# Performance work log

Measured on AMD Instinct MI355X. Metric: run time of the kernel, lower is better.

## Reference

```python
import jax, jax.numpy as jnp
import numpy as np

DIM = 768
HEADS = 12
HEAD_DIM = DIM // HEADS
EPS_ATTN = 1e-6
LN_EPS = 1e-5


def _piece_weight():
    # BlockDistanceConv with num_patches_per_side=16, patch_group_size=16 -> 4x4 blocks
    bps = 4
    centers = np.array([[i + 0.5, j + 0.5] for i in range(bps) for j in range(bps)], dtype=np.float32)
    d = np.linalg.norm(centers[:, None, :] - centers[None, :, :], axis=-1)
    mat = np.cos(d / d.max() * np.pi / 4.0)  # 'cos' transform
    mat = mat / mat.sum(axis=0, keepdims=True)
    return jnp.asarray(mat, dtype=jnp.float32)  # [16, 16], out = W @ x over piece channels


def setup_inputs() -> dict:
    key = jax.random.key(0)
    ks = jax.random.split(key, 4)
    B, N, W, C = 128, 16, 16, DIM
    x = jax.random.normal(ks[0], (B, N, W, C), dtype=jnp.float32)
    ln_gamma = jnp.ones((C,), dtype=jnp.float32)
    ln_beta = jnp.zeros((C,), dtype=jnp.float32)
    w_qkv = jax.random.normal(ks[1], (C, 3 * C), dtype=jnp.float32) * (C ** -0.5)
    w_out = jax.random.normal(ks[2], (C, C), dtype=jnp.float32) * (C ** -0.5)
    b_out = jnp.zeros((C,), dtype=jnp.float32)
    w_piece = _piece_weight()
    return {"x": x, "ln_gamma": ln_gamma, "ln_beta": ln_beta, "w_qkv": w_qkv,
            "w_out": w_out, "b_out": b_out, "w_piece": w_piece}


def reference(x, ln_gamma, ln_beta, w_qkv, w_out, b_out, w_piece):
    B, N, W, C = x.shape
    H, D = HEADS, HEAD_DIM
    # LayerNorm over channel dim
    mu = jnp.mean(x, axis=-1, keepdims=True)
    var = jnp.mean((x - mu) ** 2, axis=-1, keepdims=True)
    xn = (x - mu) * jax.lax.rsqrt(var + LN_EPS) * ln_gamma + ln_beta
    # qkv projection (no bias)
    qkv = xn @ w_qkv  # [B,N,W,3C]
    q, k, v = jnp.split(qkv, 3, axis=-1)
    # relu kernel feature map
    q = jax.nn.relu(q) + EPS_ATTN
    k = jax.nn.relu(k) + EPS_ATTN
    # split heads: 'b n w (h d) -> b h n w d'
    def heads(t):
        return t.reshape(B, N, W, H, D).transpose(0, 3, 1, 2, 4)
    q, k, v = heads(q), heads(k), heads(v)
    # per-window kv = k^T v  (sum over window positions w)  -> [B,H,N,D,D]
    kv = jnp.einsum('bhnwd,bhnwe->bhnde', k, v)
    # BlockDistanceConv: 1x1 conv mixing over piece dim N with fixed weights
    kv = jnp.einsum('ij,bhjde->bhide', w_piece, kv)
    # out = q @ kv  -> [B,H,N,W,D]
    out = jnp.einsum('bhnwd,bhnde->bhnwe', q, kv)
    # merge heads: 'b h n w d -> b n w (h d)'
    out = out.transpose(0, 2, 3, 1, 4).reshape(B, N, W, H * D)
    # output projection (dropout is identity in eval)
    return out @ w_out + b_out
```

## Files before the change

kernel.cpp:

```cpp
#include <hip/hip_runtime.h>

#define DIM 768
#define HEADS 12
#define TOK 32768

typedef unsigned short ushort_t;
typedef __attribute__((ext_vector_type(8))) short short8v;
typedef __attribute__((ext_vector_type(4))) float f32x4;
typedef __attribute__((ext_vector_type(4))) unsigned short us4;

__device__ __forceinline__ ushort_t f2bf(float x) {
  union { float f; unsigned u; } c; c.f = x;
  unsigned r = (c.u + 0x7FFFu + ((c.u >> 16) & 1u)) >> 16;
  return (ushort_t)r;
}

__device__ __forceinline__ void gload_lds16(const void* g, void* l) {
  __builtin_amdgcn_global_load_lds((const __attribute__((address_space(1))) void*)g,
                                   (__attribute__((address_space(3))) void*)l, 16, 0, 0);
}

#define FENCE asm volatile("" ::: "memory")
#define SCHED0 __builtin_amdgcn_sched_barrier(0)
#define BARRIER do { FENCE; SCHED0; __builtin_amdgcn_s_barrier(); SCHED0; FENCE; } while (0)
#define LGK0 asm volatile("s_waitcnt lgkmcnt(0)" ::: "memory")

__global__ __launch_bounds__(256) void ln_kernel(const float* __restrict__ x,
                                                 const float* __restrict__ g,
                                                 const float* __restrict__ be,
                                                 ushort_t* __restrict__ xn) {
  int lane = threadIdx.x & 63;
  int row = blockIdx.x * 4 + (threadIdx.x >> 6);
  const float4* rx = (const float4*)(x + (size_t)row * DIM);
  float4 v[3];
  float s = 0.f, sq = 0.f;
  #pragma unroll
  for (int c = 0; c < 3; ++c) {
    v[c] = rx[lane + 64 * c];
    s  += v[c].x + v[c].y + v[c].z + v[c].w;
    sq += v[c].x * v[c].x + v[c].y * v[c].y + v[c].z * v[c].z + v[c].w * v[c].w;
  }
  #pragma unroll
  for (int off = 32; off; off >>= 1) {
    s  += __shfl_xor(s, off);
    sq += __shfl_xor(sq, off);
  }
  float mu  = s * (1.0f / DIM);
  float var = sq * (1.0f / DIM) - mu * mu;
  float rs  = rsqrtf(var + 1e-5f);
  us4* orow = (us4*)(xn + (size_t)row * DIM);
  const float4* gv = (const float4*)g;
  const float4* bv = (const float4*)be;
  #pragma unroll
  for (int c = 0; c < 3; ++c) {
    float4 gg = gv[lane + 64 * c];
    float4 bb = bv[lane + 64 * c];
    us4 pk;
    pk[0] = f2bf((v[c].x - mu) * rs * gg.x + bb.x);
    pk[1] = f2bf((v[c].y - mu) * rs * gg.y + bb.y);
    pk[2] = f2bf((v[c].z - mu) * rs * gg.z + bb.z);
    pk[3] = f2bf((v[c].w - mu) * rs * gg.w + bb.w);
    orow[lane + 64 * c] = pk;
  }
}

__global__ __launch_bounds__(256) void convT2(const float* __restrict__ s0,
                                              ushort_t* __restrict__ d0,
                                              const float* __restrict__ s1,
                                              ushort_t* __restrict__ d1) {
  int z = blockIdx.z;
  if (z && blockIdx.x >= DIM / 32) return;
  const float* src = z ? s1 : s0;
  ushort_t* dst = z ? d1 : d0;
  int Ccol = z ? DIM : 3 * DIM;
  const int R = DIM;
  __shared__ float tile[32][33];
  int c0 = blockIdx.x * 32, r0 = blockIdx.y * 32;
  int tx = threadIdx.x & 31, ty = threadIdx.x >> 5;
  #pragma unroll
  for (int i = 0; i < 32; i += 8)
    tile[ty + i][tx] = src[(size_t)(r0 + ty + i) * Ccol + c0 + tx];
  __syncthreads();
  #pragma unroll
  for (int i = 0; i < 32; i += 8)
    dst[(size_t)(c0 + ty + i) * R + r0 + tx] = f2bf(tile[tx][ty + i]);
}

__global__ __launch_bounds__(512, 2) void gemm_8ph(const ushort_t* __restrict__ A,
                                                   const ushort_t* __restrict__ Bt,
                                                   ushort_t* __restrict__ qbf,
                                                   ushort_t* __restrict__ kbf,
                                                   ushort_t* __restrict__ vTbf) {
  extern __shared__ __align__(16) char lds[];
  const int Kb = DIM * 2;
  const int N = 3 * DIM;
  const int nbn = N / 256;
  const size_t GHalf = (size_t)64 * Kb;

  int bid = blockIdx.x;
  int qd = gridDim.x >> 3;
  int wid = (bid & 7) * qd + (bid >> 3);
  int bm = wid / nbn, bn = wid % nbn;
  int row0 = bm * 256, col0 = bn * 256;
  int t = threadIdx.x;
  int lane = t & 63, wave = t >> 6;
  int wr = wave >> 2, wc = wave & 3;

  const char* Ag = (const char*)A + (size_t)row0 * Kb;
  const char* Bg = (const char*)Bt + (size_t)col0 * Kb;

  int o0 = t * 16;
  int sr = o0 >> 7;
  int skb = (o0 & 127) ^ ((sr & 7) << 4);
  size_t goff = (size_t)sr * Kb + skb;

  #define STG(Gbase, Lbase, kt)                                               \
    do {                                                                      \
      gload_lds16((Gbase) + goff + (size_t)(kt) * 128, lds + (Lbase) + o0);   \
      gload_lds16((Gbase) + goff + GHalf + (size_t)(kt) * 128,                \
                  lds + (Lbase) + o0 + 8192);                                 \
    } while (0)

  int fr = lane & 15, fkb = (lane >> 4) << 4;
  int swz = (fr & 7) << 4;
  int kb0 = fkb ^ swz;
  int kb1 = (64 + fkb) ^ swz;
  int laA = (wr * 128 + fr) * 128;
  int laB = 32768 + (wc * 64 + fr) * 128;

  #define LOAD_A(dst, dbase, mq)                                              \
    _Pragma("unroll") for (int mi = 0; mi < 4; ++mi) {                        \
      dst[mi][0] = *(const short8v*)(lds + (dbase) + laA + (mq)*8192 + mi*2048 + kb0); \
      dst[mi][1] = *(const short8v*)(lds + (dbase) + laA + (mq)*8192 + mi*2048 + kb1); \
    }
  #define LOAD_B(dst, dbase, nq)                                              \
    _Pragma("unroll") for (int ni = 0; ni < 2; ++ni) {                        \
      dst[ni][0] = *(const short8v*)(lds + (dbase) + laB + (nq)*4096 + ni*2048 + kb0); \
      dst[ni][1] = *(const short8v*)(lds + (dbase) + laB + (nq)*4096 + ni*2048 + kb1); \
    }
  #define MFMA16(av, bv, mq, nq)                                              \
    do {                                                                      \
      SCHED0;                                                                 \
      __builtin_amdgcn_s_setprio(1);                                          \
      _Pragma("unroll") for (int mi = 0; mi < 4; ++mi)                        \
        _Pragma("unroll") for (int ni = 0; ni < 2; ++ni) {                    \
          acc[(mq)*4+mi][(nq)*2+ni] = __builtin_amdgcn_mfma_f32_16x16x32_bf16(\
              av[mi][0], bv[ni][0], acc[(mq)*4+mi][(nq)*2+ni], 0, 0, 0);      \
          acc[(mq)*4+mi][(nq)*2+ni] = __builtin_amdgcn_mfma_f32_16x16x32_bf16(\
              av[mi][1], bv[ni][1], acc[(mq)*4+mi][(nq)*2+ni], 0, 0, 0);      \
        }                                                                     \
      __builtin_amdgcn_s_setprio(0);                                          \
    } while (0)

  STG(Ag, 0, 0);  STG(Ag + 128 * Kb, 16384, 0);
  STG(Bg, 32768, 0);  STG(Bg + 128 * Kb, 49152, 0);
  STG(Ag, 65536, 1);  STG(Ag + 128 * Kb, 65536 + 16384, 1);
  STG(Bg, 65536 + 32768, 1);
  asm volatile("s_waitcnt vmcnt(6)" ::: "memory");
  BARRIER;

  short8v aR0[4][2], aR1[4][2], bR0[2][2], bR1[2][2];
  LOAD_A(aR0, 0, 0); LOAD_B(bR0, 0, 0);

  f32x4 acc[8][4] = {};
  for (int it = 0; it < 6; ++it) {
    const int d0 = 0, d1 = 65536;
    int t1k = 2 * it + 1, t2k = 2 * it + 2, t3k = 2 * it + 3;
    bool st = (it < 5);
    LOAD_A(aR1, d0, 1);
    STG(Bg + 128 * Kb, d1 + 49152, t1k);
    MFMA16(aR0, bR0, 0, 0);
    BARRIER;
    LOAD_B(bR1, d0, 1);
    MFMA16(aR1, bR0, 1, 0);
    BARRIER;
    if (st) { STG(Ag, d0, t2k); STG(Ag + 128 * Kb, d0 + 16384, t2k); }
    MFMA16(aR0, bR1, 0, 1);
    if (st) asm volatile("s_waitcnt vmcnt(4)" ::: "memory");
    else    asm volatile("s_waitcnt vmcnt(0)" ::: "memory");
    BARRIER;
    LOAD_A(aR0, d1, 0); LOAD_B(bR0, d1, 0);
    if (st) STG(Bg, d0 + 32768, t2k);
    MFMA16(aR1, bR1, 1, 1);
    BARRIER;
    LOAD_A(aR1, d1, 1);
    if (st) STG(Bg + 128 * Kb, d0 + 49152, t2k);
    MFMA16(aR0, bR0, 0, 0);
    BARRIER;
    LOAD_B(bR1, d1, 1);
    MFMA16(aR1, bR0, 1, 0);
    BARRIER;
    if (st) { STG(Ag, d1, t3k); STG(Ag + 128 * Kb, d1 + 16384, t3k); }
    MFMA16(aR0, bR1, 0, 1);
    if (st) asm volatile("s_waitcnt vmcnt(4)" ::: "memory");
    BARRIER;
    if (st) {
      LOAD_A(aR0, d0, 0); LOAD_B(bR0, d0, 0);
      STG(Bg, d1 + 32768, t3k);
    }
    MFMA16(aR1, bR1, 1, 1);
    BARRIER;
  }
  #undef STG
  #undef LOAD_A
  #undef LOAD_B
  #undef MFMA16

  int rbase = row0 + wr * 128 + ((lane >> 4) << 2);
  int cbase = col0 + wc * 64 + fr;
  #pragma unroll
  for (int m = 0; m < 8; ++m) {
    int r0r = rbase + m * 16;
    #pragma unroll
    for (int n = 0; n < 4; ++n) {
      int c = cbase + n * 16;
      if (c < DIM) {
        #pragma unroll
        for (int j = 0; j < 4; ++j)
          qbf[(size_t)(r0r + j) * DIM + c] = f2bf(fmaxf(acc[m][n][j], 0.0f) + 1e-6f);
      } else if (c < 2 * DIM) {
        #pragma unroll
        for (int j = 0; j < 4; ++j)
          kbf[(size_t)(r0r + j) * DIM + (c - DIM)] = f2bf(fmaxf(acc[m][n][j], 0.0f) + 1e-6f);
      } else {
        int ch = c - 2 * DIM;
        int hh = ch >> 6, e = ch & 63;
        int bb = r0r >> 8, rr = r0r & 255;
        us4 pk;
        #pragma unroll
        for (int j = 0; j < 4; ++j) pk[j] = f2bf(acc[m][n][j]);
        *(us4*)&vTbf[((((size_t)bb * HEADS + hh) * 64 + e) << 8) + rr] = pk;
      }
    }
  }
}

__global__ __launch_bounds__(512, 2) void gemm_out8(const ushort_t* __restrict__ A,
                                                    const ushort_t* __restrict__ Bt,
                                                    const float* __restrict__ bias,
                                                    float* __restrict__ C) {
  extern __shared__ __align__(16) char lds[];
  const int Kb = DIM * 2;
  const int N = DIM;
  const int nbn = N / 128;
  const size_t GHalf = (size_t)64 * Kb;

  int bid = blockIdx.x;
  int qd = gridDim.x >> 3;
  int wid = (bid & 7) * qd + (bid >> 3);
  int bm = wid / nbn, bn = wid % nbn;
  int row0 = bm * 256, col0 = bn * 128;
  int t = threadIdx.x;
  int lane = t & 63, wave = t >> 6;
  int wr = wave >> 2, wc = wave & 3;

  const char* Ag = (const char*)A + (size_t)row0 * Kb;
  const char* Bg = (const char*)Bt + (size_t)col0 * Kb;

  int o0 = t * 16;
  int sr = o0 >> 7;
  int skb = (o0 & 127) ^ ((sr & 7) << 4);
  size_t goff = (size_t)sr * Kb + skb;

  #define STGA(Gbase, Lbase, kt)                                              \
    do {                                                                      \
      gload_lds16((Gbase) + goff + (size_t)(kt) * 128, lds + (Lbase) + o0);   \
      gload_lds16((Gbase) + goff + GHalf + (size_t)(kt) * 128,                \
                  lds + (Lbase) + o0 + 8192);                                 \
    } while (0)
  #define STGB(Gbase, Lbase, kt)                                              \
    gload_lds16((Gbase) + goff + (size_t)(kt) * 128, lds + (Lbase) + o0)

  int fr = lane & 15, fkb = (lane >> 4) << 4;
  int swz = (fr & 7) << 4;
  int kb0 = fkb ^ swz;
  int kb1 = (64 + fkb) ^ swz;
  int laA = (wr * 128 + fr) * 128;
  int laB = 32768 + (wc * 32 + fr) * 128;

  #define LOAD_A(dst, dbase, mq)                                              \
    _Pragma("unroll") for (int mi = 0; mi < 4; ++mi) {                        \
      dst[mi][0] = *(const short8v*)(lds + (dbase) + laA + (mq)*8192 + mi*2048 + kb0); \
      dst[mi][1] = *(const short8v*)(lds + (dbase) + laA + (mq)*8192 + mi*2048 + kb1); \
    }
  #define LOAD_B(dst, dbase, nq)                                              \
    do {                                                                      \
      dst[0] = *(const short8v*)(lds + (dbase) + laB + (nq)*2048 + kb0);      \
      dst[1] = *(const short8v*)(lds + (dbase) + laB + (nq)*2048 + kb1);      \
    } while (0)
  #define MFMA8(av, bv, mq, nq)                                               \
    do {                                                                      \
      SCHED0;                                                                 \
      __builtin_amdgcn_s_setprio(1);                                          \
      _Pragma("unroll") for (int mi = 0; mi < 4; ++mi) {                      \
        acc[(mq)*4+mi][nq] = __builtin_amdgcn_mfma_f32_16x16x32_bf16(         \
            av[mi][0], bv[0], acc[(mq)*4+mi][nq], 0, 0, 0);                   \
        acc[(mq)*4+mi][nq] = __builtin_amdgcn_mfma_f32_16x16x32_bf16(         \
            av[mi][1], bv[1], acc[(mq)*4+mi][nq], 0, 0, 0);                   \
      }                                                                       \
      __builtin_amdgcn_s_setprio(0);                                          \
    } while (0)

  STGA(Ag, 0, 0);  STGA(Ag + 128 * Kb, 16384, 0);
  STGB(Bg, 32768, 0);  STGB(Bg + GHalf, 32768 + 8192, 0);
  STGA(Ag, 49152, 1);  STGA(Ag + 128 * Kb, 49152 + 16384, 1);
  STGB(Bg, 49152 + 32768, 1);
  asm volatile("s_waitcnt vmcnt(5)" ::: "memory");
  BARRIER;

  short8v aR0[4][2], aR1[4][2], bR0[2], bR1[2];
  LOAD_A(aR0, 0, 0); LOAD_B(bR0, 0, 0);

  f32x4 acc[8][2] = {};
  for (int it = 0; it < 6; ++it) {
    const int d0 = 0, d1 = 49152;
    int t1k = 2 * it + 1, t2k = 2 * it + 2, t3k = 2 * it + 3;
    bool st = (it < 5);
    LOAD_A(aR1, d0, 1);
    STGB(Bg + GHalf, d1 + 32768 + 8192, t1k);
    MFMA8(aR0, bR0, 0, 0);
    BARRIER;
    LOAD_B(bR1, d0, 1);
    MFMA8(aR1, bR0, 1, 0);
    BARRIER;
    if (st) { STGA(Ag, d0, t2k); STGA(Ag + 128 * Kb, d0 + 16384, t2k); }
    MFMA8(aR0, bR1, 0, 1);
    if (st) asm volatile("s_waitcnt vmcnt(4)" ::: "memory");
    else    asm volatile("s_waitcnt vmcnt(0)" ::: "memory");
    BARRIER;
    LOAD_A(aR0, d1, 0); LOAD_B(bR0, d1, 0);
    if (st) STGB(Bg, d0 + 32768, t2k);
    MFMA8(aR1, bR1, 1, 1);
    BARRIER;
    LOAD_A(aR1, d1, 1);
    if (st) STGB(Bg + GHalf, d0 + 32768 + 8192, t2k);
    MFMA8(aR0, bR0, 0, 0);
    BARRIER;
    LOAD_B(bR1, d1, 1);
    MFMA8(aR1, bR0, 1, 0);
    BARRIER;
    if (st) { STGA(Ag, d1, t3k); STGA(Ag + 128 * Kb, d1 + 16384, t3k); }
    MFMA8(aR0, bR1, 0, 1);
    if (st) asm volatile("s_waitcnt vmcnt(4)" ::: "memory");
    BARRIER;
    if (st) {
      LOAD_A(aR0, d0, 0); LOAD_B(bR0, d0, 0);
      STGB(Bg, d1 + 32768, t3k);
    }
    MFMA8(aR1, bR1, 1, 1);
    BARRIER;
  }
  #undef STGA
  #undef STGB
  #undef LOAD_A
  #undef LOAD_B
  #undef MFMA8

  int rbase = row0 + wr * 128 + ((lane >> 4) << 2);
  int cbase = col0 + wc * 32 + fr;
  #pragma unroll
  for (int m = 0; m < 8; ++m) {
    #pragma unroll
    for (int n = 0; n < 2; ++n) {
      int c = cbase + n * 16;
      float bz = bias[c];
      #pragma unroll
      for (int j = 0; j < 4; ++j)
        C[(size_t)(rbase + m * 16 + j) * N + c] = acc[m][n][j] + bz;
    }
  }
}

__global__ __launch_bounds__(512) void attn_fused(const ushort_t* __restrict__ qbf,
                                                  const ushort_t* __restrict__ kbf,
                                                  const ushort_t* __restrict__ vTbf,
                                                  const float* __restrict__ wp,
                                                  ushort_t* __restrict__ attnO) {
  extern __shared__ __align__(16) char lds[];
  const int QOFF = 65536, SOFF = 73728;
  int bh = blockIdx.x;
  int b = bh / HEADS, h = bh % HEADS;
  int t = threadIdx.x;
  int lane = t & 63, wave = t >> 6;
  int fr = lane & 15, fkb = (lane >> 4) << 4;
  int lg4 = (lane >> 4) << 2;

  const char* qg = (const char*)(qbf + ((size_t)b * 256) * DIM + h * 64);
  const char* kg = (const char*)(kbf + ((size_t)b * 256) * DIM + h * 64);
  const char* vg = (const char*)(vTbf + ((size_t)bh << 14));

  #pragma unroll
  for (int is = 0; is < 4; ++is) {
    int o = is * 8192 + t * 16;
    int r = o >> 7;
    int byt = (o & 127) ^ ((r & 7) << 4);
    gload_lds16(kg + (size_t)r * (DIM * 2) + byt, lds + o);
  }
  {
    int o = t * 16;
    int r = o >> 7;
    int byt = (o & 127) ^ ((r & 7) << 4);
    gload_lds16(qg + (size_t)r * (DIM * 2) + byt, lds + QOFF + o);
  }
  #pragma unroll
  for (int is = 0; is < 4; ++is) {
    int o = is * 8192 + t * 16;
    int e = o >> 9;
    int byt = (o & 511) ^ ((e & 7) << 4);
    gload_lds16(vg + e * 512 + byt, lds + 32768 + o);
  }
  asm volatile("s_waitcnt vmcnt(4)" ::: "memory");
  __builtin_amdgcn_s_barrier();

  int wrs = wave & 3, wcs = wave >> 2;
  int wrp = wave >> 2, wcp = wave & 3;

  for (int q4 = 0; q4 < 4; ++q4) {
    f32x4 accA[4][2] = {};
    {
      short8v kf[4][2], qf[2][2];
      #pragma unroll
      for (int mi = 0; mi < 4; ++mi)
        #pragma unroll
        for (int ks = 0; ks < 2; ++ks) {
          int r = wrs * 64 + mi * 16 + fr;
          kf[mi][ks] = *(const short8v*)(lds + r * 128 + ((ks * 64 + fkb) ^ ((r & 7) << 4)));
        }
      #pragma unroll
      for (int ni = 0; ni < 2; ++ni)
        #pragma unroll
        for (int ks = 0; ks < 2; ++ks) {
          int r = wcs * 32 + ni * 16 + fr;
          qf[ni][ks] = *(const short8v*)(lds + QOFF + r * 128 + ((ks * 64 + fkb) ^ ((r & 7) << 4)));
        }
      #pragma unroll
      for (int mi = 0; mi < 4; ++mi)
        #pragma unroll
        for (int ni = 0; ni < 2; ++ni)
          #pragma unroll
          for (int ks = 0; ks < 2; ++ks)
            accA[mi][ni] = __builtin_amdgcn_mfma_f32_16x16x32_bf16(kf[mi][ks], qf[ni][ks],
                                                                   accA[mi][ni], 0, 0, 0);
    }
    BARRIER;
    #pragma unroll
    for (int mi = 0; mi < 4; ++mi)
      #pragma unroll
      for (int ni = 0; ni < 2; ++ni) {
        float wpf = wp[(q4 * 4 + wcs * 2 + ni) * 16 + wrs * 4 + mi];
        us4 pk;
        #pragma unroll
        for (int j = 0; j < 4; ++j) pk[j] = f2bf(accA[mi][ni][j] * wpf);
        int qrow = wcs * 32 + ni * 16 + fr;
        int sbyte = (wrs * 64 + mi * 16 + lg4) * 2;
        *(us4*)(lds + SOFF + qrow * 512 + (sbyte ^ ((qrow & 7) << 4))) = pk;
      }
    if (q4 < 3) {
      int o = t * 16;
      int r = o >> 7;
      int byt = (o & 127) ^ ((r & 7) << 4);
      gload_lds16(qg + (size_t)((q4 + 1) * 64 + r) * (DIM * 2) + byt, lds + QOFF + o);
    }
    LGK0;
    BARRIER;
    if (q4 == 0) asm volatile("s_waitcnt vmcnt(1)" ::: "memory");
    f32x4 accB[2] = {{0.f,0.f,0.f,0.f},{0.f,0.f,0.f,0.f}};
    #pragma unroll
    for (int ks = 0; ks < 8; ++ks) {
      int kb = ks * 64 + fkb;
      int e = wcp * 16 + fr;
      short8v bv = *(const short8v*)(lds + 32768 + e * 512 + (kb ^ ((e & 7) << 4)));
      #pragma unroll
      for (int mt = 0; mt < 2; ++mt) {
        int r = wrp * 32 + mt * 16 + fr;
        short8v av = *(const short8v*)(lds + SOFF + r * 512 + (kb ^ ((r & 7) << 4)));
        accB[mt] = __builtin_amdgcn_mfma_f32_16x16x32_bf16(av, bv, accB[mt], 0, 0, 0);
      }
    }
    #pragma unroll
    for (int mt = 0; mt < 2; ++mt) {
      int row = b * 256 + q4 * 64 + wrp * 32 + mt * 16 + lg4;
      int col = h * 64 + wcp * 16 + fr;
      #pragma unroll
      for (int j = 0; j < 4; ++j)
        attnO[(size_t)(row + j) * DIM + col] = f2bf(accB[mt][j]);
    }
    if (q4 < 3) asm volatile("s_waitcnt vmcnt(8)" ::: "memory");
    BARRIER;
  }
}

extern "C" void kernel_launch(void* const* d_in, const int* in_sizes, int n_in,
                              void* d_out, int out_size, void* d_ws, size_t ws_size,
                              hipStream_t stream) {
  const float* x    = (const float*)d_in[0];
  const float* g    = (const float*)d_in[1];
  const float* be   = (const float*)d_in[2];
  const float* wqkv = (const float*)d_in[3];
  const float* wout = (const float*)d_in[4];
  const float* bout = (const float*)d_in[5];
  const float* wp   = (const float*)d_in[6];
  float* out = (float*)d_out;

  char* w = (char*)d_ws;
  const size_t SZ = (size_t)TOK * DIM * 2;
  ushort_t* qbf   = (ushort_t*)(w);
  ushort_t* kbf   = (ushort_t*)(w + SZ);
  ushort_t* vTbf  = (ushort_t*)(w + 2 * SZ);
  ushort_t* xn    = (ushort_t*)(w + 3 * SZ);
  ushort_t* wqkvT = (ushort_t*)(w + 4 * SZ);
  ushort_t* woutT = (ushort_t*)(w + 4 * SZ + 3538944);
  ushort_t* attnO = xn;

  (void)hipFuncSetAttribute(reinterpret_cast<const void*>(&gemm_8ph),
                            hipFuncAttributeMaxDynamicSharedMemorySize, 131072);
  (void)hipFuncSetAttribute(reinterpret_cast<const void*>(&gemm_out8),
                            hipFuncAttributeMaxDynamicSharedMemorySize, 98304);
  (void)hipFuncSetAttribute(reinterpret_cast<const void*>(&attn_fused),
                            hipFuncAttributeMaxDynamicSharedMemorySize, 106496);

  dim3 gct(3 * DIM / 32, DIM / 32, 2);
  convT2<<<gct, 256, 0, stream>>>(wqkv, wqkvT, wout, woutT);

  ln_kernel<<<TOK / 4, 256, 0, stream>>>(x, g, be, xn);

  gemm_8ph<<<(TOK / 256) * (3 * DIM / 256), 512, 131072, stream>>>(
      xn, wqkvT, qbf, kbf, vTbf);

  attn_fused<<<128 * HEADS, 512, 106496, stream>>>(qbf, kbf, vTbf, wp, attnO);

  gemm_out8<<<(TOK / 256) * (DIM / 128), 512, 98304, stream>>>(
      attnO, woutT, bout, out);
}
```

Baseline: 288.1 us.

## Reschedule GEMM main loops with finer-grained staging and explicit waitcnt barriers

Restructures the software pipeline in both GEMM kernels (QKV and output projection). Each global-to-LDS stage is now split into one load per sub-step, and every LDS fragment load is followed by a barrier and an lgkmcnt wait before the MFMA block. The prologue preloads less data, and the barrier macro no longer carries scheduling barriers, so the compiler has more freedom to reorder. The aim is to spread memory traffic evenly across MFMA phases and shorten stalls, at the cost of more barriers per iteration.

```diff
diff --git a/kernel.cpp b/kernel.cpp
--- a/kernel.cpp
+++ b/kernel.cpp
@@ -22,8 +22,11 @@
 
 #define FENCE asm volatile("" ::: "memory")
 #define SCHED0 __builtin_amdgcn_sched_barrier(0)
-#define BARRIER do { FENCE; SCHED0; __builtin_amdgcn_s_barrier(); SCHED0; FENCE; } while (0)
+#define BAR do { FENCE; __builtin_amdgcn_s_barrier(); FENCE; } while (0)
 #define LGK0 asm volatile("s_waitcnt lgkmcnt(0)" ::: "memory")
+#define LGK8 asm volatile("s_waitcnt lgkmcnt(8)" ::: "memory")
+#define VM2  asm volatile("s_waitcnt vmcnt(2)" ::: "memory")
+#define VM0  asm volatile("s_waitcnt vmcnt(0)" ::: "memory")
 
 __global__ __launch_bounds__(256) void ln_kernel(const float* __restrict__ x,
                                                  const float* __restrict__ g,
@@ -140,7 +143,6 @@
     }
   #define MFMA16(av, bv, mq, nq)                                              \
     do {                                                                      \
-      SCHED0;                                                                 \
       __builtin_amdgcn_s_setprio(1);                                          \
       _Pragma("unroll") for (int mi = 0; mi < 4; ++mi)                        \
         _Pragma("unroll") for (int ni = 0; ni < 2; ++ni) {                    \
@@ -150,56 +152,63 @@
               av[mi][1], bv[ni][1], acc[(mq)*4+mi][(nq)*2+ni], 0, 0, 0);      \
         }                                                                     \
       __builtin_amdgcn_s_setprio(0);                                          \
+      SCHED0;                                                                 \
     } while (0)
 
   STG(Ag, 0, 0);  STG(Ag + 128 * Kb, 16384, 0);
   STG(Bg, 32768, 0);  STG(Bg + 128 * Kb, 49152, 0);
-  STG(Ag, 65536, 1);  STG(Ag + 128 * Kb, 65536 + 16384, 1);
-  STG(Bg, 65536 + 32768, 1);
-  asm volatile("s_waitcnt vmcnt(6)" ::: "memory");
-  BARRIER;
-
-  short8v aR0[4][2], aR1[4][2], bR0[2][2], bR1[2][2];
-  LOAD_A(aR0, 0, 0); LOAD_B(bR0, 0, 0);
+  STG(Ag, 65536, 1);
+  VM2;
+  BAR;
 
   f32x4 acc[8][4] = {};
+  short8v A0[4][2], A1[4][2], B0[2][2], B1[2][2];
   for (int it = 0; it < 6; ++it) {
     const int d0 = 0, d1 = 65536;
-    int t1k = 2 * it + 1, t2k = 2 * it + 2, t3k = 2 * it + 3;
+    int todd = 2 * it + 1, tev = 2 * it + 2, todd3 = 2 * it + 3;
     bool st = (it < 5);
-    LOAD_A(aR1, d0, 1);
-    STG(Bg + 128 * Kb, d1 + 49152, t1k);
-    MFMA16(aR0, bR0, 0, 0);
-    BARRIER;
-    LOAD_B(bR1, d0, 1);
-    MFMA16(aR1, bR0, 1, 0);
-    BARRIER;
-    if (st) { STG(Ag, d0, t2k); STG(Ag + 128 * Kb, d0 + 16384, t2k); }
-    MFMA16(aR0, bR1, 0, 1);
-    if (st) asm volatile("s_waitcnt vmcnt(4)" ::: "memory");
-    else    asm volatile("s_waitcnt vmcnt(0)" ::: "memory");
-    BARRIER;
-    LOAD_A(aR0, d1, 0); LOAD_B(bR0, d1, 0);
-    if (st) STG(Bg, d0 + 32768, t2k);
-    MFMA16(aR1, bR1, 1, 1);
-    BARRIER;
-    LOAD_A(aR1, d1, 1);
-    if (st) STG(Bg + 128 * Kb, d0 + 49152, t2k);
-    MFMA16(aR0, bR0, 0, 0);
-    BARRIER;
-    LOAD_B(bR1, d1, 1);
-    MFMA16(aR1, bR0, 1, 0);
-    BARRIER;
-    if (st) { STG(Ag, d1, t3k); STG(Ag + 128 * Kb, d1 + 16384, t3k); }
-    MFMA16(aR0, bR1, 0, 1);
-    if (st) asm volatile("s_waitcnt vmcnt(4)" ::: "memory");
-    BARRIER;
-    if (st) {
-      LOAD_A(aR0, d0, 0); LOAD_B(bR0, d0, 0);
-      STG(Bg, d1 + 32768, t3k);
-    }
-    MFMA16(aR1, bR1, 1, 1);
-    BARRIER;
+    LOAD_A(A0, d0, 0); LOAD_B(B0, d0, 0);
+    STG(Ag + 128 * Kb, d1 + 16384, todd);
+    LGK8;
+    BAR; LGK0; SCHED0;
+    MFMA16(A0, B0, 0, 0);
+    BAR;
+    LOAD_A(A1, d0, 1);
+    STG(Bg, d1 + 32768, todd);
+    BAR; LGK0; SCHED0;
+    MFMA16(A1, B0, 1, 0);
+    BAR;
+    LOAD_B(B1, d0, 1);
+    STG(Bg + 128 * Kb, d1 + 49152, todd);
+    BAR; LGK0; SCHED0;
+    MFMA16(A0, B1, 0, 1);
+    BAR;
+    if (st) STG(Ag, d0, tev);
+    BAR; SCHED0;
+    MFMA16(A1, B1, 1, 1);
+    if (st) VM2; else VM0;
+    BAR;
+    LOAD_A(A0, d1, 0); LOAD_B(B0, d1, 0);
+    if (st) STG(Ag + 128 * Kb, d0 + 16384, tev);
+    LGK8;
+    BAR; LGK0; SCHED0;
+    MFMA16(A0, B0, 0, 0);
+    BAR;
+    LOAD_A(A1, d1, 1);
+    if (st) STG(Bg, d0 + 32768, tev);
+    BAR; LGK0; SCHED0;
+    MFMA16(A1, B0, 1, 0);
+    BAR;
+    LOAD_B(B1, d1, 1);
+    if (st) STG(Bg + 128 * Kb, d0 + 49152, tev);
+    BAR; LGK0; SCHED0;
+    MFMA16(A0, B1, 0, 1);
+    BAR;
+    if (st) STG(Ag, d1, todd3);
+    BAR; SCHED0;
+    MFMA16(A1, B1, 1, 1);
+    if (st) VM2;
+    BAR;
   }
   #undef STG
   #undef LOAD_A
@@ -290,7 +299,6 @@
     } while (0)
   #define MFMA8(av, bv, mq, nq)                                               \
     do {                                                                      \
-      SCHED0;                                                                 \
       __builtin_amdgcn_s_setprio(1);                                          \
       _Pragma("unroll") for (int mi = 0; mi < 4; ++mi) {                      \
         acc[(mq)*4+mi][nq] = __builtin_amdgcn_mfma_f32_16x16x32_bf16(         \
@@ -299,56 +307,61 @@
             av[mi][1], bv[1], acc[(mq)*4+mi][nq], 0, 0, 0);                   \
       }                                                                       \
       __builtin_amdgcn_s_setprio(0);                                          \
+      SCHED0;                                                                 \
     } while (0)
 
   STGA(Ag, 0, 0);  STGA(Ag + 128 * Kb, 16384, 0);
-  STGB(Bg, 32768, 0);  STGB(Bg + GHalf, 32768 + 8192, 0);
-  STGA(Ag, 49152, 1);  STGA(Ag + 128 * Kb, 49152 + 16384, 1);
-  STGB(Bg, 49152 + 32768, 1);
-  asm volatile("s_waitcnt vmcnt(5)" ::: "memory");
-  BARRIER;
-
-  short8v aR0[4][2], aR1[4][2], bR0[2], bR1[2];
-  LOAD_A(aR0, 0, 0); LOAD_B(bR0, 0, 0);
+  STGB(Bg, 32768, 0);  STGB(Bg + GHalf, 40960, 0);
+  STGA(Ag, 49152, 1);
+  VM2;
+  BAR;
 
   f32x4 acc[8][2] = {};
+  short8v A0[4][2], A1[4][2], B0[2], B1[2];
   for (int it = 0; it < 6; ++it) {
     const int d0 = 0, d1 = 49152;
-    int t1k = 2 * it + 1, t2k = 2 * it + 2, t3k = 2 * it + 3;
+    int todd = 2 * it + 1, tev = 2 * it + 2, todd3 = 2 * it + 3;
     bool st = (it < 5);
-    LOAD_A(aR1, d0, 1);
-    STGB(Bg + GHalf, d1 + 32768 + 8192, t1k);
-    MFMA8(aR0, bR0, 0, 0);
-    BARRIER;
-    LOAD_B(bR1, d0, 1);
-    MFMA8(aR1, bR0, 1, 0);
-    BARRIER;
-    if (st) { STGA(Ag, d0, t2k); STGA(Ag + 128 * Kb, d0 + 16384, t2k); }
-    MFMA8(aR0, bR1, 0, 1);
-    if (st) asm volatile("s_waitcnt vmcnt(4)" ::: "memory");
-    else    asm volatile("s_waitcnt vmcnt(0)" ::: "memory");
-    BARRIER;
-    LOAD_A(aR0, d1, 0); LOAD_B(bR0, d1, 0);
-    if (st) STGB(Bg, d0 + 32768, t2k);
-    MFMA8(aR1, bR1, 1, 1);
-    BARRIER;
-    LOAD_A(aR1, d1, 1);
-    if (st) STGB(Bg + GHalf, d0 + 32768 + 8192, t2k);
-    MFMA8(aR0, bR0, 0, 0);
-    BARRIER;
-    LOAD_B(bR1, d1, 1);
-    MFMA8(aR1, bR0, 1, 0);
-    BARRIER;
-    if (st) { STGA(Ag, d1, t3k); STGA(Ag + 128 * Kb, d1 + 16384, t3k); }
-    MFMA8(aR0, bR1, 0, 1);
-    if (st) asm volatile("s_waitcnt vmcnt(4)" ::: "memory");
-    BARRIER;
-    if (st) {
-      LOAD_A(aR0, d0, 0); LOAD_B(bR0, d0, 0);
-      STGB(Bg, d1 + 32768, t3k);
-    }
-    MFMA8(aR1, bR1, 1, 1);
-    BARRIER;
+    LOAD_A(A0, d0, 0); LOAD_B(B0, d0, 0);
+    STGA(Ag + 128 * Kb, d1 + 16384, todd);
+    BAR; LGK0; SCHED0;
+    MFMA8(A0, B0, 0, 0);
+    BAR;
+    LOAD_A(A1, d0, 1);
+    STGB(Bg, d1 + 32768, todd);
+    BAR; LGK0; SCHED0;
+    MFMA8(A1, B0, 1, 0);
+    BAR;
+    LOAD_B(B1, d0, 1);
+    STGB(Bg + GHalf, d1 + 40960, todd);
+    BAR; LGK0; SCHED0;
+    MFMA8(A0, B1, 0, 1);
+    BAR;
+    if (st) STGA(Ag, d0, tev);
+    BAR; SCHED0;
+    MFMA8(A1, B1, 1, 1);
+    if (st) VM2; else VM0;
+    BAR;
+    LOAD_A(A0, d1, 0); LOAD_B(B0, d1, 0);
+    if (st) STGA(Ag + 128 * Kb, d0 + 16384, tev);
+    BAR; LGK0; SCHED0;
+    MFMA8(A0, B0, 0, 0);
+    BAR;
+    LOAD_A(A1, d1, 1);
+    if (st) STGB(Bg, d0 + 32768, tev);
+    BAR; LGK0; SCHED0;
+    MFMA8(A1, B0, 1, 0);
+    BAR;
+    LOAD_B(B1, d1, 1);
+    if (st) STGB(Bg + GHalf, d0 + 40960, tev);
+    BAR; LGK0; SCHED0;
+    MFMA8(A0, B1, 0, 1);
+    BAR;
+    if (st) STGA(Ag, d1, todd3);
+    BAR; SCHED0;
+    MFMA8(A1, B1, 1, 1);
+    if (st) VM2;
+    BAR;
   }
   #undef STGA
   #undef STGB
@@ -442,7 +455,7 @@
             accA[mi][ni] = __builtin_amdgcn_mfma_f32_16x16x32_bf16(kf[mi][ks], qf[ni][ks],
                                                                    accA[mi][ni], 0, 0, 0);
     }
-    BARRIER;
+    BAR;
     #pragma unroll
     for (int mi = 0; mi < 4; ++mi)
       #pragma unroll
@@ -462,7 +475,7 @@
       gload_lds16(qg + (size_t)((q4 + 1) * 64 + r) * (DIM * 2) + byt, lds + QOFF + o);
     }
     LGK0;
-    BARRIER;
+    BAR;
     if (q4 == 0) asm volatile("s_waitcnt vmcnt(1)" ::: "memory");
     f32x4 accB[2] = {{0.f,0.f,0.f,0.f},{0.f,0.f,0.f,0.f}};
     #pragma unroll
@@ -486,7 +499,7 @@
         attnO[(size_t)(row + j) * DIM + col] = f2bf(accB[mt][j]);
     }
     if (q4 < 3) asm volatile("s_waitcnt vmcnt(8)" ::: "memory");
-    BARRIER;
+    BAR;
   }
 }
 
```

After: 290.6 us. Within noise of the previous version (+0.9%).

## Shrink LDS footprint of output GEMM and attention kernels to raise occupancy

Applied to the files above, without the earlier changes.

The output GEMM drops its hand-tuned 8-phase, 128-byte-K pipeline for a simple double-buffered loop over 32-wide K tiles using 48KB of LDS, with a 4x2 wave grid holding 4x4 accumulators each and launch bounds asking for 4 blocks per CU. The attention kernel keeps V^T in registers, reusing the V LDS region as score scratch so its LDS shrinks to 72KB, and also asks for 4 blocks per CU. The goal is more resident blocks to hide latency, at the cost of losing the finer software pipelining, adding more barriers per K step and increasing register pressure.

```diff
diff --git a/kernel.cpp b/kernel.cpp
--- a/kernel.cpp
+++ b/kernel.cpp
@@ -24,6 +24,8 @@
 #define SCHED0 __builtin_amdgcn_sched_barrier(0)
 #define BARRIER do { FENCE; SCHED0; __builtin_amdgcn_s_barrier(); SCHED0; FENCE; } while (0)
 #define LGK0 asm volatile("s_waitcnt lgkmcnt(0)" ::: "memory")
+#define VM0  asm volatile("s_waitcnt vmcnt(0)" ::: "memory")
+#define VM3  asm volatile("s_waitcnt vmcnt(3)" ::: "memory")
 
 __global__ __launch_bounds__(256) void ln_kernel(const float* __restrict__ x,
                                                  const float* __restrict__ g,
@@ -235,7 +237,7 @@
   }
 }
 
-__global__ __launch_bounds__(512, 2) void gemm_out8(const ushort_t* __restrict__ A,
+__global__ __launch_bounds__(512, 4) void gemm_out8(const ushort_t* __restrict__ A,
                                                     const ushort_t* __restrict__ Bt,
                                                     const float* __restrict__ bias,
                                                     float* __restrict__ C) {
@@ -243,7 +245,7 @@
   const int Kb = DIM * 2;
   const int N = DIM;
   const int nbn = N / 128;
-  const size_t GHalf = (size_t)64 * Kb;
+  const int NT = DIM / 32;
 
   int bid = blockIdx.x;
   int qd = gridDim.x >> 3;
@@ -252,116 +254,65 @@
   int row0 = bm * 256, col0 = bn * 128;
   int t = threadIdx.x;
   int lane = t & 63, wave = t >> 6;
-  int wr = wave >> 2, wc = wave & 3;
+  int wr = wave >> 1, wc = wave & 1;
 
   const char* Ag = (const char*)A + (size_t)row0 * Kb;
   const char* Bg = (const char*)Bt + (size_t)col0 * Kb;
 
-  int o0 = t * 16;
-  int sr = o0 >> 7;
-  int skb = (o0 & 127) ^ ((sr & 7) << 4);
-  size_t goff = (size_t)sr * Kb + skb;
-
-  #define STGA(Gbase, Lbase, kt)                                              \
+  int oA0 = t * 16, oA1 = 8192 + t * 16;
+  int rA0 = oA0 >> 6, rA1 = oA1 >> 6;
+  size_t gA0 = (size_t)rA0 * Kb + ((oA0 & 63) ^ ((rA0 & 3) << 4));
+  size_t gA1 = (size_t)rA1 * Kb + ((oA1 & 63) ^ ((rA1 & 3) << 4));
+  int oB = t * 16;
+  int rB = oB >> 6;
+  size_t gB = (size_t)rB * Kb + ((oB & 63) ^ ((rB & 3) << 4));
+
+  #define STG2(tile, slot)                                                    \
     do {                                                                      \
-      gload_lds16((Gbase) + goff + (size_t)(kt) * 128, lds + (Lbase) + o0);   \
-      gload_lds16((Gbase) + goff + GHalf + (size_t)(kt) * 128,                \
-                  lds + (Lbase) + o0 + 8192);                                 \
+      char* sb = lds + (slot) * 24576;                                        \
+      size_t kk = (size_t)(tile) * 64;                                        \
+      gload_lds16(Ag + gA0 + kk, sb + oA0);                                   \
+      gload_lds16(Ag + gA1 + kk, sb + oA1);                                   \
+      gload_lds16(Bg + gB + kk, sb + 16384 + oB);                             \
     } while (0)
-  #define STGB(Gbase, Lbase, kt)                                              \
-    gload_lds16((Gbase) + goff + (size_t)(kt) * 128, lds + (Lbase) + o0)
 
   int fr = lane & 15, fkb = (lane >> 4) << 4;
-  int swz = (fr & 7) << 4;
-  int kb0 = fkb ^ swz;
-  int kb1 = (64 + fkb) ^ swz;
-  int laA = (wr * 128 + fr) * 128;
-  int laB = 32768 + (wc * 32 + fr) * 128;
-
-  #define LOAD_A(dst, dbase, mq)                                              \
-    _Pragma("unroll") for (int mi = 0; mi < 4; ++mi) {                        \
-      dst[mi][0] = *(const short8v*)(lds + (dbase) + laA + (mq)*8192 + mi*2048 + kb0); \
-      dst[mi][1] = *(const short8v*)(lds + (dbase) + laA + (mq)*8192 + mi*2048 + kb1); \
-    }
-  #define LOAD_B(dst, dbase, nq)                                              \
-    do {                                                                      \
-      dst[0] = *(const short8v*)(lds + (dbase) + laB + (nq)*2048 + kb0);      \
-      dst[1] = *(const short8v*)(lds + (dbase) + laB + (nq)*2048 + kb1);      \
-    } while (0)
-  #define MFMA8(av, bv, mq, nq)                                               \
-    do {                                                                      \
-      SCHED0;                                                                 \
-      __builtin_amdgcn_s_setprio(1);                                          \
-      _Pragma("unroll") for (int mi = 0; mi < 4; ++mi) {                      \
-        acc[(mq)*4+mi][nq] = __builtin_amdgcn_mfma_f32_16x16x32_bf16(         \
-            av[mi][0], bv[0], acc[(mq)*4+mi][nq], 0, 0, 0);                   \
-        acc[(mq)*4+mi][nq] = __builtin_amdgcn_mfma_f32_16x16x32_bf16(         \
-            av[mi][1], bv[1], acc[(mq)*4+mi][nq], 0, 0, 0);                   \
-      }                                                                       \
-      __builtin_amdgcn_s_setprio(0);                                          \
-    } while (0)
-
-  STGA(Ag, 0, 0);  STGA(Ag + 128 * Kb, 16384, 0);
-  STGB(Bg, 32768, 0);  STGB(Bg + GHalf, 32768 + 8192, 0);
-  STGA(Ag, 49152, 1);  STGA(Ag + 128 * Kb, 49152 + 16384, 1);
-  STGB(Bg, 49152 + 32768, 1);
-  asm volatile("s_waitcnt vmcnt(5)" ::: "memory");
-  BARRIER;
-
-  short8v aR0[4][2], aR1[4][2], bR0[2], bR1[2];
-  LOAD_A(aR0, 0, 0); LOAD_B(bR0, 0, 0);
-
-  f32x4 acc[8][2] = {};
-  for (int it = 0; it < 6; ++it) {
-    const int d0 = 0, d1 = 49152;
-    int t1k = 2 * it + 1, t2k = 2 * it + 2, t3k = 2 * it + 3;
-    bool st = (it < 5);
-    LOAD_A(aR1, d0, 1);
-    STGB(Bg + GHalf, d1 + 32768 + 8192, t1k);
-    MFMA8(aR0, bR0, 0, 0);
-    BARRIER;
-    LOAD_B(bR1, d0, 1);
-    MFMA8(aR1, bR0, 1, 0);
-    BARRIER;
-    if (st) { STGA(Ag, d0, t2k); STGA(Ag + 128 * Kb, d0 + 16384, t2k); }
-    MFMA8(aR0, bR1, 0, 1);
-    if (st) asm volatile("s_waitcnt vmcnt(4)" ::: "memory");
-    else    asm volatile("s_waitcnt vmcnt(0)" ::: "memory");
-    BARRIER;
-    LOAD_A(aR0, d1, 0); LOAD_B(bR0, d1, 0);
-    if (st) STGB(Bg, d0 + 32768, t2k);
-    MFMA8(aR1, bR1, 1, 1);
-    BARRIER;
-    LOAD_A(aR1, d1, 1);
-    if (st) STGB(Bg + GHalf, d0 + 32768 + 8192, t2k);
-    MFMA8(aR0, bR0, 0, 0);
-    BARRIER;
-    LOAD_B(bR1, d1, 1);
-    MFMA8(aR1, bR0, 1, 0);
-    BARRIER;
-    if (st) { STGA(Ag, d1, t3k); STGA(Ag + 128 * Kb, d1 + 16384, t3k); }
-    MFMA8(aR0, bR1, 0, 1);
-    if (st) asm volatile("s_waitcnt vmcnt(4)" ::: "memory");
-    BARRIER;
-    if (st) {
-      LOAD_A(aR0, d0, 0); LOAD_B(bR0, d0, 0);
-      STGB(Bg, d1 + 32768, t3k);
-    }
-    MFMA8(aR1, bR1, 1, 1);
-    BARRIER;
-  }
-  #undef STGA
-  #undef STGB
-  #undef LOAD_A
-  #undef LOAD_B
-  #undef MFMA8
-
-  int rbase = row0 + wr * 128 + ((lane >> 4) << 2);
-  int cbase = col0 + wc * 32 + fr;
-  #pragma unroll
-  for (int m = 0; m < 8; ++m) {
-    #pragma unroll
-    for (int n = 0; n < 2; ++n) {
+  int kb = fkb ^ ((fr & 3) << 4);
+  int aoff = (wr * 64 + fr) * 64 + kb;
+  int boff = 16384 + (wc * 64 + fr) * 64 + kb;
+
+  STG2(0, 0);
+
+  f32x4 acc[4][4] = {};
+  for (int kt = 0; kt < NT; ++kt) {
+    int cur = kt & 1;
+    if (kt + 1 < NT) { STG2(kt + 1, cur ^ 1); VM3; }
+    else VM0;
+    BARRIER;
+    const char* sb = lds + cur * 24576;
+    short8v a[4], b[4];
+    #pragma unroll
+    for (int mi = 0; mi < 4; ++mi) a[mi] = *(const short8v*)(sb + aoff + mi * 1024);
+    #pragma unroll
+    for (int ni = 0; ni < 4; ++ni) b[ni] = *(const short8v*)(sb + boff + ni * 1024);
+    SCHED0;
+    __builtin_amdgcn_s_setprio(1);
+    #pragma unroll
+    for (int mi = 0; mi < 4; ++mi)
+      #pragma unroll
+      for (int ni = 0; ni < 4; ++ni)
+        acc[mi][ni] = __builtin_amdgcn_mfma_f32_16x16x32_bf16(a[mi], b[ni], acc[mi][ni], 0, 0, 0);
+    __builtin_amdgcn_s_setprio(0);
+    BARRIER;
+  }
+  #undef STG2
+
+  int rbase = row0 + wr * 64 + ((lane >> 4) << 2);
+  int cbase = col0 + wc * 64 + fr;
+  #pragma unroll
+  for (int m = 0; m < 4; ++m) {
+    #pragma unroll
+    for (int n = 0; n < 4; ++n) {
       int c = cbase + n * 16;
       float bz = bias[c];
       #pragma unroll
@@ -371,13 +322,13 @@
   }
 }
 
-__global__ __launch_bounds__(512) void attn_fused(const ushort_t* __restrict__ qbf,
-                                                  const ushort_t* __restrict__ kbf,
-                                                  const ushort_t* __restrict__ vTbf,
-                                                  const float* __restrict__ wp,
-                                                  ushort_t* __restrict__ attnO) {
+__global__ __launch_bounds__(512, 4) void attn_fused(const ushort_t* __restrict__ qbf,
+                                                     const ushort_t* __restrict__ kbf,
+                                                     const ushort_t* __restrict__ vTbf,
+                                                     const float* __restrict__ wp,
+                                                     ushort_t* __restrict__ attnO) {
   extern __shared__ __align__(16) char lds[];
-  const int QOFF = 65536, SOFF = 73728;
+  const int QOFF = 32768, SOFF = 40960;
   int bh = blockIdx.x;
   int b = bh / HEADS, h = bh % HEADS;
   int t = threadIdx.x;
@@ -407,40 +358,48 @@
     int o = is * 8192 + t * 16;
     int e = o >> 9;
     int byt = (o & 511) ^ ((e & 7) << 4);
-    gload_lds16(vg + e * 512 + byt, lds + 32768 + o);
-  }
-  asm volatile("s_waitcnt vmcnt(4)" ::: "memory");
+    gload_lds16(vg + e * 512 + byt, lds + SOFF + o);
+  }
+  VM0;
   __builtin_amdgcn_s_barrier();
 
   int wrs = wave & 3, wcs = wave >> 2;
   int wrp = wave >> 2, wcp = wave & 3;
+
+  short8v vt[8];
+  {
+    int e = wcp * 16 + fr;
+    int es = (e & 7) << 4;
+    #pragma unroll
+    for (int ks = 0; ks < 8; ++ks)
+      vt[ks] = *(const short8v*)(lds + SOFF + e * 512 + ((ks * 64 + fkb) ^ es));
+  }
+  LGK0;
+  BARRIER;
 
   for (int q4 = 0; q4 < 4; ++q4) {
     f32x4 accA[4][2] = {};
     {
-      short8v kf[4][2], qf[2][2];
-      #pragma unroll
-      for (int mi = 0; mi < 4; ++mi)
+      short8v qf[2][2];
+      #pragma unroll
+      for (int ni = 0; ni < 2; ++ni) {
+        int r = wcs * 32 + ni * 16 + fr;
+        int rs = (r & 7) << 4;
+        qf[ni][0] = *(const short8v*)(lds + QOFF + r * 128 + (fkb ^ rs));
+        qf[ni][1] = *(const short8v*)(lds + QOFF + r * 128 + ((64 + fkb) ^ rs));
+      }
+      #pragma unroll
+      for (int mi = 0; mi < 4; ++mi) {
+        int r = wrs * 64 + mi * 16 + fr;
+        int rs = (r & 7) << 4;
+        short8v kf0 = *(const short8v*)(lds + r * 128 + (fkb ^ rs));
+        short8v kf1 = *(const short8v*)(lds + r * 128 + ((64 + fkb) ^ rs));
         #pragma unroll
-        for (int ks = 0; ks < 2; ++ks) {
-          int r = wrs * 64 + mi * 16 + fr;
-          kf[mi][ks] = *(const short8v*)(lds + r * 128 + ((ks * 64 + fkb) ^ ((r & 7) << 4)));
+        for (int ni = 0; ni < 2; ++ni) {
+          accA[mi][ni] = __builtin_amdgcn_mfma_f32_16x16x32_bf16(kf0, qf[ni][0], accA[mi][ni], 0, 0, 0);
+          accA[mi][ni] = __builtin_amdgcn_mfma_f32_16x16x32_bf16(kf1, qf[ni][1], accA[mi][ni], 0, 0, 0);
         }
-      #pragma unroll
-      for (int ni = 0; ni < 2; ++ni)
-        #pragma unroll
-        for (int ks = 0; ks < 2; ++ks) {
-          int r = wcs * 32 + ni * 16 + fr;
-          qf[ni][ks] = *(const short8v*)(lds + QOFF + r * 128 + ((ks * 64 + fkb) ^ ((r & 7) << 4)));
-        }
-      #pragma unroll
-      for (int mi = 0; mi < 4; ++mi)
-        #pragma unroll
-        for (int ni = 0; ni < 2; ++ni)
-          #pragma unroll
-          for (int ks = 0; ks < 2; ++ks)
-            accA[mi][ni] = __builtin_amdgcn_mfma_f32_16x16x32_bf16(kf[mi][ks], qf[ni][ks],
-                                                                   accA[mi][ni], 0, 0, 0);
+      }
     }
     BARRIER;
     #pragma unroll
@@ -463,18 +422,15 @@
     }
     LGK0;
     BARRIER;
-    if (q4 == 0) asm volatile("s_waitcnt vmcnt(1)" ::: "memory");
     f32x4 accB[2] = {{0.f,0.f,0.f,0.f},{0.f,0.f,0.f,0.f}};
     #pragma unroll
     for (int ks = 0; ks < 8; ++ks) {
-      int kb = ks * 64 + fkb;
-      int e = wcp * 16 + fr;
-      short8v bv = *(const short8v*)(lds + 32768 + e * 512 + (kb ^ ((e & 7) << 4)));
+      int kbq = ks * 64 + fkb;
       #pragma unroll
       for (int mt = 0; mt < 2; ++mt) {
         int r = wrp * 32 + mt * 16 + fr;
-        short8v av = *(const short8v*)(lds + SOFF + r * 512 + (kb ^ ((r & 7) << 4)));
-        accB[mt] = __builtin_amdgcn_mfma_f32_16x16x32_bf16(av, bv, accB[mt], 0, 0, 0);
+        short8v av = *(const short8v*)(lds + SOFF + r * 512 + (kbq ^ ((r & 7) << 4)));
+        accB[mt] = __builtin_amdgcn_mfma_f32_16x16x32_bf16(av, vt[ks], accB[mt], 0, 0, 0);
       }
     }
     #pragma unroll
@@ -515,9 +471,9 @@
   (void)hipFuncSetAttribute(reinterpret_cast<const void*>(&gemm_8ph),
                             hipFuncAttributeMaxDynamicSharedMemorySize, 131072);
   (void)hipFuncSetAttribute(reinterpret_cast<const void*>(&gemm_out8),
-                            hipFuncAttributeMaxDynamicSharedMemorySize, 98304);
+                            hipFuncAttributeMaxDynamicSharedMemorySize, 49152);
   (void)hipFuncSetAttribute(reinterpret_cast<const void*>(&attn_fused),
-                            hipFuncAttributeMaxDynamicSharedMemorySize, 106496);
+                            hipFuncAttributeMaxDynamicSharedMemorySize, 73728);
 
   dim3 gct(3 * DIM / 32, DIM / 32, 2);
   convT2<<<gct, 256, 0, stream>>>(wqkv, wqkvT, wout, woutT);
@@ -527,8 +483,8 @@
   gemm_8ph<<<(TOK / 256) * (3 * DIM / 256), 512, 131072, stream>>>(
       xn, wqkvT, qbf, kbf, vTbf);
 
-  attn_fused<<<128 * HEADS, 512, 106496, stream>>>(qbf, kbf, vTbf, wp, attnO);
-
-  gemm_out8<<<(TOK / 256) * (DIM / 128), 512, 98304, stream>>>(
+  attn_fused<<<128 * HEADS, 512, 73728, stream>>>(qbf, kbf, vTbf, wp, attnO);
+
+  gemm_out8<<<(TOK / 256) * (DIM / 128), 512, 49152, stream>>>(
       attnO, woutT, bout, out);
 }
```

Result: faster. 269.1 us (-6.6%).
